# Kernel tuning notes

Hardware: AMD Instinct MI355X
Metric: run time of the kernel (lower is better)

Reference implementation:

```python
import jax, jax.numpy as jnp
import numpy as np

D = 1024
H = 16
DK = D // H
SCALE = 1.0 / jnp.sqrt(jnp.float32(DK))


def setup_inputs() -> dict:
    key0 = jax.random.key(0)
    ks = jax.random.split(key0, 11)
    B, S = 2, 2048
    std = 1.0 / np.sqrt(D)
    inp = {
        "query": jax.random.normal(ks[0], (B, S, D), jnp.float32),
        "key": jax.random.normal(ks[1], (B, S, D), jnp.float32),
        "value": jax.random.normal(ks[2], (B, S, D), jnp.float32),
        "wq": jax.random.normal(ks[3], (D, D), jnp.float32) * std,
        "bq": jax.random.normal(ks[4], (D,), jnp.float32) * std,
        "wk": jax.random.normal(ks[5], (D, D), jnp.float32) * std,
        "bk": jax.random.normal(ks[6], (D,), jnp.float32) * std,
        "wv": jax.random.normal(ks[7], (D, D), jnp.float32) * std,
        "bv": jax.random.normal(ks[8], (D,), jnp.float32) * std,
        "wo": jax.random.normal(ks[9], (D, D), jnp.float32) * std,
        "bo": jax.random.normal(ks[10], (D,), jnp.float32) * std,
    }
    return inp


def _split_heads(x):
    # [B,S,D] -> [B,H,S,dk]
    B, S, _ = x.shape
    return x.reshape(B, S, H, DK).transpose(0, 2, 1, 3)


def reference(query, key, value, wq, bq, wk, bk, wv, bv, wo, bo):
    B, S, _ = query.shape
    # Linear projections (torch nn.Linear: x @ W^T + b)
    q = _split_heads(query @ wq.T + bq)
    k = _split_heads(key @ wk.T + bk)
    v = _split_heads(value @ wv.T + bv)
    # Scaled dot-product attention scores [B,H,S,S]
    scores = jnp.einsum("bhqd,bhkd->bhqk", q * SCALE, k)
    attention = jax.nn.softmax(scores, axis=-1)
    # Dropout in eval mode == identity
    out = jnp.einsum("bhqk,bhkd->bhqd", attention, v)
    out = out.transpose(0, 2, 1, 3).reshape(B, S, D)
    out = out @ wo.T + bo
    return out, attention
```

## Files before the change

### kernel.cpp

```cpp
#include <hip/hip_runtime.h>
#include <stdint.h>

typedef __attribute__((ext_vector_type(4))) float f32x4;
typedef __attribute__((ext_vector_type(8))) short short8;

#define MFMA16(a, b, c) __builtin_amdgcn_mfma_f32_16x16x32_bf16((a), (b), (c), 0, 0, 0)
#define EXP2(x) __builtin_amdgcn_exp2f(x)
#define LOG2(x) __builtin_amdgcn_logf(x)

__device__ __forceinline__ unsigned short f2bf(float f) {
  unsigned int x = __float_as_uint(f);
  return (unsigned short)((x + 0x7fffu + ((x >> 16) & 1u)) >> 16);
}

__device__ __forceinline__ unsigned int cvtpk(float lo, float hi) {
  unsigned int d;
  asm("v_cvt_pk_bf16_f32 %0, %1, %2" : "=v"(d) : "v"(lo), "v"(hi));
  return d;
}

__device__ __forceinline__ void gl2lds16(const void* g, void* l) {
  __builtin_amdgcn_global_load_lds((const __attribute__((address_space(1))) void*)g,
                                   (__attribute__((address_space(3))) void*)l, 16, 0, 0);
}

__device__ __forceinline__ void load8cv(const float* __restrict__ s, void* d) {
  const f32x4* p = (const f32x4*)s;
  f32x4 a = p[0], b = p[1];
  short8 t;
  t[0] = (short)f2bf(a[0]); t[1] = (short)f2bf(a[1]);
  t[2] = (short)f2bf(a[2]); t[3] = (short)f2bf(a[3]);
  t[4] = (short)f2bf(b[0]); t[5] = (short)f2bf(b[1]);
  t[6] = (short)f2bf(b[2]); t[7] = (short)f2bf(b[3]);
  *(short8*)d = t;
}

#define ENT_V0 asm volatile("s_waitcnt vmcnt(0)\ns_barrier" ::: "memory")
#define ENT_V4 asm volatile("s_waitcnt vmcnt(4)\ns_barrier" ::: "memory")

__global__ __launch_bounds__(256) void cast_all(const float* __restrict__ wq,
                                                const float* __restrict__ wk,
                                                const float* __restrict__ wv,
                                                const float* __restrict__ wo,
                                                const float* __restrict__ q_in,
                                                const float* __restrict__ k_in,
                                                const float* __restrict__ v_in,
                                                unsigned short* __restrict__ W16,
                                                unsigned short* __restrict__ Qin,
                                                unsigned short* __restrict__ Kin,
                                                unsigned short* __restrict__ Vin) {
  int i = blockIdx.x * 256 + threadIdx.x;
  if (i < 524288) {
    int which = i >> 17;
    int off = (i & 131071) * 8;
    const float* src = which == 0 ? wq : which == 1 ? wk : which == 2 ? wv : wo;
    load8cv(src + off, W16 + (size_t)which * 1048576 + off);
  } else {
    int j = i - 524288;
    int which = j >> 19;
    int off = (j & 524287) * 8;
    const float* src = which == 0 ? q_in : which == 1 ? k_in : v_in;
    unsigned short* dst = which == 0 ? Qin : which == 1 ? Kin : Vin;
    load8cv(src + off, dst + off);
  }
}

__global__ __launch_bounds__(256) void qkv_proj(const unsigned short* __restrict__ Qin,
                                                const unsigned short* __restrict__ Kin,
                                                const unsigned short* __restrict__ Vin,
                                                const unsigned short* __restrict__ W16,
                                                const float* __restrict__ bq,
                                                const float* __restrict__ bk,
                                                const float* __restrict__ bv,
                                                unsigned short* __restrict__ Q16,
                                                unsigned short* __restrict__ K16,
                                                unsigned short* __restrict__ V16) {
  const int z = blockIdx.z;
  const unsigned short* A = z == 0 ? Qin : z == 1 ? Kin : Vin;
  const unsigned short* Bt = W16 + (size_t)z * 1048576;
  const float* bias = z == 0 ? bq : z == 1 ? bk : bv;
  unsigned short* C = z == 0 ? Q16 : z == 1 ? K16 : V16;
  const float oscale = z == 0 ? 0.18033688f : 1.0f;
  const int K = 1024, N = 1024;

  __shared__ __align__(16) char lds[32768];
  char* As = lds;
  char* Bs = lds + 16384;
  const int tid = threadIdx.x;
  const int lane = tid & 63;
  const int wv = tid >> 6;
  const int g = lane >> 4, r = lane & 15;
  const int wm = wv >> 1, wn = wv & 1;
  const int m0 = blockIdx.y * 128, n0 = blockIdx.x * 128;

  f32x4 acc[4][4];
#pragma unroll
  for (int m = 0; m < 4; ++m)
#pragma unroll
    for (int n = 0; n < 4; ++n) acc[m][n] = (f32x4){0.f, 0.f, 0.f, 0.f};

  for (int k0 = 0; k0 < K; k0 += 64) {
    __syncthreads();
#pragma unroll
    for (int i = 0; i < 4; ++i) {
      int c = (wv * 4 + i) * 64 + lane;
      int row = c >> 3;
      gl2lds16(Bt + (size_t)(n0 + row) * K + k0 + (c & 7) * 8, Bs + (wv * 4 + i) * 1024);
    }
#pragma unroll
    for (int i = 0; i < 4; ++i) {
      int c = (wv * 4 + i) * 64 + lane;
      int row = c >> 3;
      gl2lds16(A + (size_t)(m0 + row) * K + k0 + (c & 7) * 8, As + (wv * 4 + i) * 1024);
    }
    __syncthreads();
#pragma unroll
    for (int kk = 0; kk < 2; ++kk) {
      short8 af[4], bfr[4];
#pragma unroll
      for (int m = 0; m < 4; ++m)
        af[m] = *(const short8*)(As + (wm * 64 + m * 16 + r) * 128 + kk * 64 + g * 16);
#pragma unroll
      for (int n = 0; n < 4; ++n)
        bfr[n] = *(const short8*)(Bs + (wn * 64 + n * 16 + r) * 128 + kk * 64 + g * 16);
#pragma unroll
      for (int m = 0; m < 4; ++m)
#pragma unroll
        for (int n = 0; n < 4; ++n) acc[m][n] = MFMA16(af[m], bfr[n], acc[m][n]);
    }
  }

#pragma unroll
  for (int n = 0; n < 4; ++n) {
    int col = n0 + wn * 64 + n * 16 + r;
    float bv_ = bias[col];
#pragma unroll
    for (int m = 0; m < 4; ++m)
#pragma unroll
      for (int i = 0; i < 4; ++i) {
        int rowg = m0 + wm * 64 + m * 16 + 4 * g + i;
        C[(size_t)rowg * N + col] = f2bf((acc[m][n][i] + bv_) * oscale);
      }
  }
}

__global__ __launch_bounds__(256) void o_proj(const unsigned short* __restrict__ A,
                                              const unsigned short* __restrict__ Bt,
                                              const float* __restrict__ bias,
                                              float* __restrict__ C) {
  const int K = 1024, N = 1024;
  __shared__ __align__(16) char lds[24576];
  char* As = lds;
  char* Bs = lds + 16384;
  const int tid = threadIdx.x;
  const int lane = tid & 63;
  const int wv = tid >> 6;
  const int g = lane >> 4, r = lane & 15;
  const int wm = wv >> 1, wn = wv & 1;
  const int m0 = blockIdx.y * 128, n0 = blockIdx.x * 64;

  f32x4 acc[4][2];
#pragma unroll
  for (int m = 0; m < 4; ++m)
#pragma unroll
    for (int n = 0; n < 2; ++n) acc[m][n] = (f32x4){0.f, 0.f, 0.f, 0.f};

  for (int k0 = 0; k0 < K; k0 += 64) {
    __syncthreads();
#pragma unroll
    for (int i = 0; i < 2; ++i) {
      int c = (wv * 2 + i) * 64 + lane;
      int row = c >> 3;
      gl2lds16(Bt + (size_t)(n0 + row) * K + k0 + (c & 7) * 8, Bs + (wv * 2 + i) * 1024);
    }
#pragma unroll
    for (int i = 0; i < 4; ++i) {
      int c = (wv * 4 + i) * 64 + lane;
      int row = c >> 3;
      gl2lds16(A + (size_t)(m0 + row) * K + k0 + (c & 7) * 8, As + (wv * 4 + i) * 1024);
    }
    __syncthreads();
#pragma unroll
    for (int kk = 0; kk < 2; ++kk) {
      short8 af[4], bfr[2];
#pragma unroll
      for (int m = 0; m < 4; ++m)
        af[m] = *(const short8*)(As + (wm * 64 + m * 16 + r) * 128 + kk * 64 + g * 16);
#pragma unroll
      for (int n = 0; n < 2; ++n)
        bfr[n] = *(const short8*)(Bs + (wn * 32 + n * 16 + r) * 128 + kk * 64 + g * 16);
#pragma unroll
      for (int m = 0; m < 4; ++m)
#pragma unroll
        for (int n = 0; n < 2; ++n) acc[m][n] = MFMA16(af[m], bfr[n], acc[m][n]);
    }
  }

#pragma unroll
  for (int n = 0; n < 2; ++n) {
    int col = n0 + wn * 32 + n * 16 + r;
    float bv_ = bias[col];
#pragma unroll
    for (int m = 0; m < 4; ++m)
#pragma unroll
      for (int i = 0; i < 4; ++i) {
        int rowg = m0 + wm * 64 + m * 16 + 4 * g + i;
        C[(size_t)rowg * N + col] = acc[m][n][i] + bv_;
      }
  }
}

__global__ __launch_bounds__(256) void transpose_v(const unsigned short* __restrict__ V,
                                                   unsigned short* __restrict__ Vt) {
  int t = blockIdx.x * 256 + threadIdx.x;
  int d = t & 63;
  int sc = (t >> 6) & 255;
  int bh = t >> 14;
  int b = bh >> 4, h = bh & 15;
  unsigned short vals[8];
#pragma unroll
  for (int j = 0; j < 8; ++j)
    vals[j] = V[(size_t)(b * 2048 + sc * 8 + j) * 1024 + h * 64 + d];
  *(short8*)&Vt[((size_t)bh * 64 + d) * 2048 + sc * 8] = *(short8*)vals;
}

__global__ __launch_bounds__(256, 4) void attn_fused(const unsigned short* __restrict__ Q,
                                                     const unsigned short* __restrict__ K,
                                                     const unsigned short* __restrict__ Vt,
                                                     float* __restrict__ attn,
                                                     unsigned short* __restrict__ O) {
  __shared__ __align__(16) char lds[32768];
  const int tid = threadIdx.x;
  const int lane = tid & 63;
  const int wv = tid >> 6;
  const int g = lane >> 4, r = lane & 15;
  int nb = (blockIdx.x & 7) * 128 + (blockIdx.x >> 3);
  const int qt = nb & 31, bh = nb >> 5, h = bh & 15, b = bh >> 4;
  const int qloc = qt * 64 + wv * 16;
  const int qrow0 = b * 2048 + qloc;
  const unsigned short* Kbh = K + (size_t)b * 2048 * 1024 + h * 64;
  const unsigned short* Vbh = Vt + (size_t)bh * 64 * 2048;
  float* attn_bh = attn + (size_t)bh * 2048 * 2048;

  short8 qf[2];
#pragma unroll
  for (int kk = 0; kk < 2; ++kk)
    qf[kk] = *(const short8*)&Q[(size_t)(qrow0 + r) * 1024 + h * 64 + kk * 32 + g * 8];

#define P1_ISSUE(bb, ktt)                                                      \
  do {                                                                         \
    _Pragma("unroll") for (int i_ = 0; i_ < 4; ++i_) {                         \
      int c_ = (wv * 4 + i_) * 64 + lane;                                      \
      int kr_ = c_ >> 3;                                                       \
      int scb_ = ((c_ & 7) * 16) ^ ((kr_ & 7) << 4);                           \
      gl2lds16(Kbh + (size_t)((ktt) + kr_) * 1024 + (scb_ >> 1),               \
               (bb) + (wv * 4 + i_) * 1024);                                   \
    }                                                                          \
  } while (0)
#define P2_ISSUE(bb, ktt)                                                      \
  do {                                                                         \
    _Pragma("unroll") for (int i_ = 0; i_ < 4; ++i_) {                         \
      int c_ = (wv * 4 + i_) * 64 + lane;                                      \
      int kr_ = (c_ >> 3) & 63;                                                \
      int scb_ = ((c_ & 7) * 16) ^ ((kr_ & 7) << 4);                           \
      const unsigned short* src_ =                                             \
          (c_ < 512) ? (Kbh + (size_t)((ktt) + kr_) * 1024 + (scb_ >> 1))      \
                     : (Vbh + (size_t)kr_ * 2048 + (ktt) + (scb_ >> 1));       \
      gl2lds16(src_, (bb) + (wv * 4 + i_) * 1024);                             \
    }                                                                          \
  } while (0)

  float lrow = 0.f;
  int cur = 0;
  P1_ISSUE(lds, 0);
  for (int t = 0; t < 16; ++t) {
    char* bcur = lds + (cur << 14);
    ENT_V0;
    if (t < 15) P1_ISSUE(lds + ((cur ^ 1) << 14), (t + 1) * 128);
#pragma unroll
    for (int ct = 0; ct < 8; ++ct) {
      int row = ct * 16 + r;
      int sw = (row & 7) << 4;
      short8 kf0 = *(const short8*)(bcur + ((row * 128 + g * 16) ^ sw));
      short8 kf1 = *(const short8*)(bcur + ((row * 128 + 64 + g * 16) ^ sw));
      f32x4 s = (f32x4){0.f, 0.f, 0.f, 0.f};
      s = MFMA16(kf0, qf[0], s);
      s = MFMA16(kf1, qf[1], s);
      lrow += (EXP2(s[0]) + EXP2(s[1])) + (EXP2(s[2]) + EXP2(s[3]));
    }
    cur ^= 1;
  }
  lrow += __shfl_xor(lrow, 16);
  lrow += __shfl_xor(lrow, 32);
  const float negml = -LOG2(lrow);
  const f32x4 cinit = (f32x4){negml, negml, negml, negml};

  f32x4 oacc[4];
#pragma unroll
  for (int i = 0; i < 4; ++i) oacc[i] = (f32x4){0.f, 0.f, 0.f, 0.f};

  float* arow = attn_bh + (size_t)(qloc + r) * 2048 + 4 * g;
  cur = 0;
  P2_ISSUE(lds, 0);
  for (int t = 0; t < 32; ++t) {
    char* bcur = lds + (cur << 14);
    int kt = t * 64;
    if (t == 0) {
      ENT_V0;
    } else {
      ENT_V4;
    }
    if (t < 31) P2_ISSUE(lds + ((cur ^ 1) << 14), kt + 64);
    unsigned w[4][2];
#pragma unroll
    for (int ct = 0; ct < 4; ++ct) {
      int row = ct * 16 + r;
      int sw = (row & 7) << 4;
      short8 kf0 = *(const short8*)(bcur + ((row * 128 + g * 16) ^ sw));
      short8 kf1 = *(const short8*)(bcur + ((row * 128 + 64 + g * 16) ^ sw));
      f32x4 s = MFMA16(kf0, qf[0], cinit);
      s = MFMA16(kf1, qf[1], s);
      f32x4 p;
      p[0] = EXP2(s[0]); p[1] = EXP2(s[1]);
      p[2] = EXP2(s[2]); p[3] = EXP2(s[3]);
      __builtin_nontemporal_store(p, (f32x4*)(arow + kt + 16 * ct));
      w[ct][0] = cvtpk(p[0], p[1]);
      w[ct][1] = cvtpk(p[2], p[3]);
    }
    __builtin_amdgcn_s_setprio(1);
#pragma unroll
    for (int kk2 = 0; kk2 < 2; ++kk2) {
      unsigned x0 = w[2 * kk2][0], y0 = w[2 * kk2 + 1][0];
      unsigned x1 = w[2 * kk2][1], y1 = w[2 * kk2 + 1][1];
      asm("v_permlane32_swap_b32 %0, %1" : "+v"(x0), "+v"(y0));
      asm("v_permlane16_swap_b32 %0, %1" : "+v"(x0), "+v"(y0));
      asm("v_permlane32_swap_b32 %0, %1" : "+v"(x1), "+v"(y1));
      asm("v_permlane16_swap_b32 %0, %1" : "+v"(x1), "+v"(y1));
      union { unsigned u[4]; short8 v8; } pau;
      pau.u[0] = x0; pau.u[1] = x1; pau.u[2] = y0; pau.u[3] = y1;
      short8 pa = pau.v8;
#pragma unroll
      for (int ct2 = 0; ct2 < 4; ++ct2) {
        int vrow = ct2 * 16 + r;
        short8 vf = *(const short8*)(bcur + 8192 +
                                     ((vrow * 128 + kk2 * 64 + g * 16) ^ ((vrow & 7) << 4)));
        oacc[ct2] = MFMA16(pa, vf, oacc[ct2]);
      }
    }
    __builtin_amdgcn_s_setprio(0);
    cur ^= 1;
  }
#pragma unroll
  for (int ct2 = 0; ct2 < 4; ++ct2)
#pragma unroll
    for (int i = 0; i < 4; ++i)
      O[(size_t)(qrow0 + 4 * g + i) * 1024 + h * 64 + ct2 * 16 + r] = f2bf(oacc[ct2][i]);
#undef P1_ISSUE
#undef P2_ISSUE
}

extern "C" void kernel_launch(void* const* d_in, const int* in_sizes, int n_in,
                              void* d_out, int out_size, void* d_ws, size_t ws_size,
                              hipStream_t stream) {
  const float* q_in = (const float*)d_in[0];
  const float* k_in = (const float*)d_in[1];
  const float* v_in = (const float*)d_in[2];
  const float* wq = (const float*)d_in[3];
  const float* bq = (const float*)d_in[4];
  const float* wk = (const float*)d_in[5];
  const float* bk = (const float*)d_in[6];
  const float* wv = (const float*)d_in[7];
  const float* bv = (const float*)d_in[8];
  const float* wo = (const float*)d_in[9];
  const float* bo = (const float*)d_in[10];

  char* ws = (char*)d_ws;
  const size_t MB8 = 8ull * 1024 * 1024;
  unsigned short* W16 = (unsigned short*)(ws);
  unsigned short* Qin = (unsigned short*)(ws + MB8);
  unsigned short* Kin = (unsigned short*)(ws + 2 * MB8);
  unsigned short* Vin = (unsigned short*)(ws + 3 * MB8);
  unsigned short* Q16 = (unsigned short*)(ws + 4 * MB8);
  unsigned short* K16 = (unsigned short*)(ws + 5 * MB8);
  unsigned short* V16 = (unsigned short*)(ws + 6 * MB8);
  unsigned short* Vt  = (unsigned short*)(ws + 7 * MB8);
  unsigned short* O16 = (unsigned short*)(ws + 6 * MB8);

  float* out = (float*)d_out;
  float* attn = out + 4194304ull;

  dim3 blk(256);
  cast_all<<<dim3(8192), blk, 0, stream>>>(wq, wk, wv, wo, q_in, k_in, v_in, W16, Qin, Kin, Vin);
  qkv_proj<<<dim3(8, 32, 3), blk, 0, stream>>>(Qin, Kin, Vin, W16, bq, bk, bv, Q16, K16, V16);
  transpose_v<<<dim3(2048), blk, 0, stream>>>(V16, Vt);
  attn_fused<<<dim3(1024), blk, 0, stream>>>(Q16, K16, Vt, attn, O16);
  o_proj<<<dim3(16, 32), blk, 0, stream>>>(O16, W16 + 3145728, bo, out);
}
```

Before: 269.4 us.

## Fuse V transpose into QKV projection epilogue and widen o_proj tiles

The V projection now writes its output directly in transposed [b,h,d,s] layout from the GEMM epilogue, using packed bf16 stores, so the separate transpose_v kernel and its extra global round trip are removed. The o_proj GEMM tile is widened from 128x64 to 128x128, which doubles the accumulators per wave and halves the grid. The workspace layout is adjusted so O16 no longer aliases the V buffer. The risks are lower occupancy in o_proj and the transposed V stores, which are 8-byte strided writes rather than coalesced rows.

Result: no change. 271.3 us (+0.7%).

```diff
diff --git a/kernel.cpp b/kernel.cpp
--- a/kernel.cpp
+++ b/kernel.cpp
@@ -3,6 +3,7 @@
 
 typedef __attribute__((ext_vector_type(4))) float f32x4;
 typedef __attribute__((ext_vector_type(8))) short short8;
+typedef __attribute__((ext_vector_type(2))) unsigned int u32x2;
 
 #define MFMA16(a, b, c) __builtin_amdgcn_mfma_f32_16x16x32_bf16((a), (b), (c), 0, 0, 0)
 #define EXP2(x) __builtin_amdgcn_exp2f(x)
@@ -74,12 +75,11 @@
                                                 const float* __restrict__ bv,
                                                 unsigned short* __restrict__ Q16,
                                                 unsigned short* __restrict__ K16,
-                                                unsigned short* __restrict__ V16) {
+                                                unsigned short* __restrict__ Vt) {
   const int z = blockIdx.z;
   const unsigned short* A = z == 0 ? Qin : z == 1 ? Kin : Vin;
   const unsigned short* Bt = W16 + (size_t)z * 1048576;
   const float* bias = z == 0 ? bq : z == 1 ? bk : bv;
-  unsigned short* C = z == 0 ? Q16 : z == 1 ? K16 : V16;
   const float oscale = z == 0 ? 0.18033688f : 1.0f;
   const int K = 1024, N = 1024;
 
@@ -130,17 +130,38 @@
     }
   }
 
-#pragma unroll
-  for (int n = 0; n < 4; ++n) {
-    int col = n0 + wn * 64 + n * 16 + r;
-    float bv_ = bias[col];
-#pragma unroll
-    for (int m = 0; m < 4; ++m)
-#pragma unroll
-      for (int i = 0; i < 4; ++i) {
-        int rowg = m0 + wm * 64 + m * 16 + 4 * g + i;
-        C[(size_t)rowg * N + col] = f2bf((acc[m][n][i] + bv_) * oscale);
+  if (z == 2) {
+    const int b_ = m0 >> 11;
+    const int s0 = (m0 & 2047) + wm * 64;
+#pragma unroll
+    for (int n = 0; n < 4; ++n) {
+      int col = n0 + wn * 64 + n * 16 + r;
+      int h_ = col >> 6, d_ = col & 63;
+      float bv_ = bias[col];
+      unsigned short* vtb = Vt + ((size_t)(b_ * 16 + h_) * 64 + d_) * 2048;
+#pragma unroll
+      for (int m = 0; m < 4; ++m) {
+        int s_ = s0 + m * 16 + 4 * g;
+        u32x2 pk;
+        pk[0] = cvtpk(acc[m][n][0] + bv_, acc[m][n][1] + bv_);
+        pk[1] = cvtpk(acc[m][n][2] + bv_, acc[m][n][3] + bv_);
+        *(u32x2*)(vtb + s_) = pk;
       }
+    }
+  } else {
+    unsigned short* C = z == 0 ? Q16 : K16;
+#pragma unroll
+    for (int n = 0; n < 4; ++n) {
+      int col = n0 + wn * 64 + n * 16 + r;
+      float bv_ = bias[col];
+#pragma unroll
+      for (int m = 0; m < 4; ++m)
+#pragma unroll
+        for (int i = 0; i < 4; ++i) {
+          int rowg = m0 + wm * 64 + m * 16 + 4 * g + i;
+          C[(size_t)rowg * N + col] = f2bf((acc[m][n][i] + bv_) * oscale);
+        }
+    }
   }
 }
 
@@ -149,7 +170,7 @@
                                               const float* __restrict__ bias,
                                               float* __restrict__ C) {
   const int K = 1024, N = 1024;
-  __shared__ __align__(16) char lds[24576];
+  __shared__ __align__(16) char lds[32768];
   char* As = lds;
   char* Bs = lds + 16384;
   const int tid = threadIdx.x;
@@ -157,21 +178,21 @@
   const int wv = tid >> 6;
   const int g = lane >> 4, r = lane & 15;
   const int wm = wv >> 1, wn = wv & 1;
-  const int m0 = blockIdx.y * 128, n0 = blockIdx.x * 64;
-
-  f32x4 acc[4][2];
+  const int m0 = blockIdx.y * 128, n0 = blockIdx.x * 128;
+
+  f32x4 acc[4][4];
 #pragma unroll
   for (int m = 0; m < 4; ++m)
 #pragma unroll
-    for (int n = 0; n < 2; ++n) acc[m][n] = (f32x4){0.f, 0.f, 0.f, 0.f};
+    for (int n = 0; n < 4; ++n) acc[m][n] = (f32x4){0.f, 0.f, 0.f, 0.f};
 
   for (int k0 = 0; k0 < K; k0 += 64) {
     __syncthreads();
 #pragma unroll
-    for (int i = 0; i < 2; ++i) {
-      int c = (wv * 2 + i) * 64 + lane;
+    for (int i = 0; i < 4; ++i) {
+      int c = (wv * 4 + i) * 64 + lane;
       int row = c >> 3;
-      gl2lds16(Bt + (size_t)(n0 + row) * K + k0 + (c & 7) * 8, Bs + (wv * 2 + i) * 1024);
+      gl2lds16(Bt + (size_t)(n0 + row) * K + k0 + (c & 7) * 8, Bs + (wv * 4 + i) * 1024);
     }
 #pragma unroll
     for (int i = 0; i < 4; ++i) {
@@ -182,23 +203,23 @@
     __syncthreads();
 #pragma unroll
     for (int kk = 0; kk < 2; ++kk) {
-      short8 af[4], bfr[2];
+      short8 af[4], bfr[4];
 #pragma unroll
       for (int m = 0; m < 4; ++m)
         af[m] = *(const short8*)(As + (wm * 64 + m * 16 + r) * 128 + kk * 64 + g * 16);
 #pragma unroll
-      for (int n = 0; n < 2; ++n)
-        bfr[n] = *(const short8*)(Bs + (wn * 32 + n * 16 + r) * 128 + kk * 64 + g * 16);
+      for (int n = 0; n < 4; ++n)
+        bfr[n] = *(const short8*)(Bs + (wn * 64 + n * 16 + r) * 128 + kk * 64 + g * 16);
 #pragma unroll
       for (int m = 0; m < 4; ++m)
 #pragma unroll
-        for (int n = 0; n < 2; ++n) acc[m][n] = MFMA16(af[m], bfr[n], acc[m][n]);
-    }
-  }
-
-#pragma unroll
-  for (int n = 0; n < 2; ++n) {
-    int col = n0 + wn * 32 + n * 16 + r;
+        for (int n = 0; n < 4; ++n) acc[m][n] = MFMA16(af[m], bfr[n], acc[m][n]);
+    }
+  }
+
+#pragma unroll
+  for (int n = 0; n < 4; ++n) {
+    int col = n0 + wn * 64 + n * 16 + r;
     float bv_ = bias[col];
 #pragma unroll
     for (int m = 0; m < 4; ++m)
@@ -208,20 +229,6 @@
         C[(size_t)rowg * N + col] = acc[m][n][i] + bv_;
       }
   }
-}
-
-__global__ __launch_bounds__(256) void transpose_v(const unsigned short* __restrict__ V,
-                                                   unsigned short* __restrict__ Vt) {
-  int t = blockIdx.x * 256 + threadIdx.x;
-  int d = t & 63;
-  int sc = (t >> 6) & 255;
-  int bh = t >> 14;
-  int b = bh >> 4, h = bh & 15;
-  unsigned short vals[8];
-#pragma unroll
-  for (int j = 0; j < 8; ++j)
-    vals[j] = V[(size_t)(b * 2048 + sc * 8 + j) * 1024 + h * 64 + d];
-  *(short8*)&Vt[((size_t)bh * 64 + d) * 2048 + sc * 8] = *(short8*)vals;
 }
 
 __global__ __launch_bounds__(256, 4) void attn_fused(const unsigned short* __restrict__ Q,
@@ -382,17 +389,15 @@
   unsigned short* Vin = (unsigned short*)(ws + 3 * MB8);
   unsigned short* Q16 = (unsigned short*)(ws + 4 * MB8);
   unsigned short* K16 = (unsigned short*)(ws + 5 * MB8);
-  unsigned short* V16 = (unsigned short*)(ws + 6 * MB8);
-  unsigned short* Vt  = (unsigned short*)(ws + 7 * MB8);
-  unsigned short* O16 = (unsigned short*)(ws + 6 * MB8);
+  unsigned short* Vt  = (unsigned short*)(ws + 6 * MB8);
+  unsigned short* O16 = (unsigned short*)(ws + 7 * MB8);
 
   float* out = (float*)d_out;
   float* attn = out + 4194304ull;
 
   dim3 blk(256);
   cast_all<<<dim3(8192), blk, 0, stream>>>(wq, wk, wv, wo, q_in, k_in, v_in, W16, Qin, Kin, Vin);
-  qkv_proj<<<dim3(8, 32, 3), blk, 0, stream>>>(Qin, Kin, Vin, W16, bq, bk, bv, Q16, K16, V16);
-  transpose_v<<<dim3(2048), blk, 0, stream>>>(V16, Vt);
+  qkv_proj<<<dim3(8, 32, 3), blk, 0, stream>>>(Qin, Kin, Vin, W16, bq, bk, bv, Q16, K16, Vt);
   attn_fused<<<dim3(1024), blk, 0, stream>>>(Q16, K16, Vt, attn, O16);
-  o_proj<<<dim3(16, 32), blk, 0, stream>>>(O16, W16 + 3145728, bo, out);
-}
+  o_proj<<<dim3(8, 32), blk, 0, stream>>>(O16, W16 + 3145728, bo, out);
+}
```
